# Kernel tuning notes

Measured on AMD Instinct MI355X. Metric: run time of the kernel, lower is better.

The kernel has to match this reference:

```python
import jax, jax.numpy as jnp
import numpy as np

N = 50000
E = 800000
NODE_F = 128
HID = 96
TEMP_F = 10


def setup_inputs() -> dict:
    key = jax.random.key(0)
    ks = jax.random.split(key, 10)
    x = jax.random.normal(ks[0], (N, NODE_F), dtype=jnp.float32)
    edge_index = jax.random.randint(ks[1], (2, E), 0, N, dtype=jnp.int64)
    temporal = jax.random.normal(ks[2], (N, TEMP_F), dtype=jnp.float32)
    # GCNConv: lin weight [in, out] (no bias in lin), separate bias [out]
    W_gcn = jax.random.normal(ks[3], (NODE_F, HID), dtype=jnp.float32) / np.sqrt(NODE_F)
    b_gcn = jnp.zeros((HID,), dtype=jnp.float32)
    W1 = jax.random.normal(ks[4], (HID + TEMP_F, HID), dtype=jnp.float32) / np.sqrt(HID + TEMP_F)
    b1 = jax.random.normal(ks[5], (HID,), dtype=jnp.float32) * 0.01
    W2 = jax.random.normal(ks[6], (HID + NODE_F, 1), dtype=jnp.float32) / np.sqrt(HID + NODE_F)
    b2 = jax.random.normal(ks[7], (1,), dtype=jnp.float32) * 0.01
    return {"x": x, "edge_index": edge_index, "temporal": temporal,
            "W_gcn": W_gcn, "b_gcn": b_gcn, "W1": W1, "b1": b1, "W2": W2, "b2": b2}


def _gcn_conv(x, edge_index, W, b):
    n = x.shape[0]
    loop = jnp.arange(n, dtype=edge_index.dtype)
    src = jnp.concatenate([edge_index[0], loop])  # [E+N]
    dst = jnp.concatenate([edge_index[1], loop])
    # symmetric normalization with self-loops (PyG gcn_norm)
    ones = jnp.ones(src.shape[0], dtype=x.dtype)
    deg = jax.ops.segment_sum(ones, dst, num_segments=n)
    dinv = jnp.where(deg > 0, jax.lax.rsqrt(deg), 0.0)
    norm = dinv[src] * dinv[dst]  # [E+N]
    h = x @ W  # [N, HID]
    msg = h[src] * norm[:, None]  # [E+N, HID] gather + scale
    out = jax.ops.segment_sum(msg, dst, num_segments=n)  # scatter-add
    return out + b


def reference(x, edge_index, temporal, W_gcn, b_gcn, W1, b1, W2, b2):
    h = jax.nn.relu(_gcn_conv(x, edge_index, W_gcn, b_gcn))  # [N, HID]
    h = jnp.concatenate([h, temporal], axis=-1)              # [N, HID+TEMP_F]
    h = jax.nn.relu(h @ W1 + b1)                             # [N, HID]
    h = jnp.concatenate([h, x], axis=-1)                     # [N, HID+NODE_F]
    return jax.nn.relu(h @ W2 + b2)                          # [N, 1]
```

## Files before the change

### kernel.cpp

```cpp
#include <hip/hip_runtime.h>
#include <hip/hip_bf16.h>

#define NN 50000
#define NPAD 50048
#define NE 800000
#define NF 128
#define HH 96
#define TF 10
#define Z1DIM (HH + TF)
#define ZK 128
#define NCH 4
#define CW 24
#define NBK 196
#define CAP 5120
#define EPB 8192

typedef __attribute__((ext_vector_type(8))) short short8;
typedef __attribute__((ext_vector_type(4))) float f32x4;

__device__ __forceinline__ float bu2f(unsigned short u) {
    union { unsigned int i; float f; } c;
    c.i = ((unsigned int)u) << 16;
    return c.f;
}
__device__ __forceinline__ unsigned short f2bu(float f) {
    union { __hip_bfloat16 h; unsigned short u; } c;
    c.h = __float2bfloat16(f);
    return c.u;
}

__global__ void k_init(int* __restrict__ bcur) {
    int t = threadIdx.x;
    if (t < NBK) bcur[t] = t * CAP;
}

__global__ __launch_bounds__(256) void k_fillA(const int* __restrict__ ei,
                                               int* __restrict__ bcur,
                                               int* __restrict__ temp) {
    __shared__ int hist[NBK], base[NBK];
    const int t = threadIdx.x;
    for (int m = t; m < NBK; m += 256) hist[m] = 0;
    __syncthreads();
    const int e0 = blockIdx.x * EPB;
    const int ecap = min(e0 + EPB, NE);
    for (int e = e0 + t; e < ecap; e += 256) {
        int d = ei[NE + e];
        atomicAdd(&hist[d >> 8], 1);
    }
    __syncthreads();
    for (int m = t; m < NBK; m += 256) {
        int c = hist[m];
        base[m] = c ? atomicAdd(&bcur[m], c) : 0;
        hist[m] = 0;
    }
    __syncthreads();
    for (int e = e0 + t; e < ecap; e += 256) {
        int d = ei[NE + e], s = ei[e];
        int b = d >> 8;
        int r = atomicAdd(&hist[b], 1);
        temp[base[b] + r] = ((d & 255) << 16) | s;
    }
}

__global__ __launch_bounds__(256) void k_gscan(const int* __restrict__ bcur,
                                               int* __restrict__ gbase) {
    __shared__ int p[256];
    const int t = threadIdx.x;
    int sz = (t < NBK) ? (bcur[t] - t * CAP) : 0;
    p[t] = sz;
    __syncthreads();
#pragma unroll
    for (int d = 1; d < 256; d <<= 1) {
        int u = (t >= d) ? p[t - d] : 0;
        __syncthreads();
        p[t] += u;
        __syncthreads();
    }
    if (t < NBK) gbase[t] = p[t] - sz;
}

__global__ __launch_bounds__(256) void k_fillB(const int* __restrict__ temp,
                                               const int* __restrict__ bcur,
                                               const int* __restrict__ gbase,
                                               int* __restrict__ csr,
                                               int* __restrict__ cnt,
                                               int* __restrict__ off,
                                               float* __restrict__ dinv) {
    __shared__ int ls[256], lc[256];
    const int b = blockIdx.x, t = threadIdx.x;
    const int seg0 = b * CAP;
    const int m = bcur[b] - seg0;
    const int g0 = gbase[b];
    ls[t] = 0;
    __syncthreads();
    for (int k = t; k < m; k += 256) atomicAdd(&ls[temp[seg0 + k] >> 16], 1);
    __syncthreads();
    const int myc = ls[t];
    lc[t] = myc;
    __syncthreads();
#pragma unroll
    for (int d = 1; d < 256; d <<= 1) {
        int u = (t >= d) ? lc[t - d] : 0;
        __syncthreads();
        lc[t] += u;
        __syncthreads();
    }
    const int myoff = lc[t] - myc;
    __syncthreads();
    lc[t] = myoff;
    const int i = b * 256 + t;
    if (i < NN) {
        cnt[i] = myc;
        off[i] = g0 + myoff;
        dinv[i] = rsqrtf((float)myc + 1.0f);
    }
    __syncthreads();
    for (int k = t; k < m; k += 256) {
        int v = temp[seg0 + k];
        int r = atomicAdd(&lc[v >> 16], 1);
        csr[g0 + r] = v & 0xFFFF;
    }
}

#define XBLK (NPAD * NF / 4 / 256)
#define WBLK (NF * HH / 4 / 256)
#define W1BLK (HH * ZK / 4 / 256)
__global__ void k_prep(const float* __restrict__ x, const float* __restrict__ W,
                       const float* __restrict__ W1,
                       unsigned short* __restrict__ xb, unsigned short* __restrict__ Wt,
                       unsigned short* __restrict__ Wt1) {
    int b = blockIdx.x;
    if (b < XBLK) {
        int idx4 = (b * 256 + threadIdx.x) * 4;
        int row = idx4 >> 7;
        ushort4 v;
        if (row < NN) {
            float4 f = *(const float4*)(x + idx4);
            v.x = f2bu(f.x); v.y = f2bu(f.y); v.z = f2bu(f.z); v.w = f2bu(f.w);
        } else {
            v.x = v.y = v.z = v.w = 0;
        }
        *(ushort4*)(xb + idx4) = v;
    } else if (b < XBLK + WBLK) {
        int e = ((b - XBLK) * 256 + threadIdx.x) * 4;
        int n = e >> 7, k = e & 127;
        ushort4 v;
        v.x = f2bu(W[(k + 0) * HH + n]);
        v.y = f2bu(W[(k + 1) * HH + n]);
        v.z = f2bu(W[(k + 2) * HH + n]);
        v.w = f2bu(W[(k + 3) * HH + n]);
        *(ushort4*)(Wt + e) = v;
    } else {
        int e = ((b - XBLK - WBLK) * 256 + threadIdx.x) * 4;
        int n = e >> 7, k = e & 127;
        ushort4 v;
        v.x = (k + 0 < Z1DIM) ? f2bu(W1[(k + 0) * HH + n]) : (unsigned short)0;
        v.y = (k + 1 < Z1DIM) ? f2bu(W1[(k + 1) * HH + n]) : (unsigned short)0;
        v.z = (k + 2 < Z1DIM) ? f2bu(W1[(k + 2) * HH + n]) : (unsigned short)0;
        v.w = (k + 3 < Z1DIM) ? f2bu(W1[(k + 3) * HH + n]) : (unsigned short)0;
        *(ushort4*)(Wt1 + e) = v;
    }
}

__global__ __launch_bounds__(256) void k_gemm(const unsigned short* __restrict__ xb,
                                              const unsigned short* __restrict__ Wt,
                                              const float* __restrict__ dinv,
                                              unsigned short* __restrict__ hp_c) {
    const int wave = threadIdx.x >> 6;
    const int lane = threadIdx.x & 63;
    const int quad = lane >> 4;
    const int l16 = lane & 15;
    const int Mbase = blockIdx.x * 64 + wave * 16;

    const unsigned short* arow = xb + (size_t)(Mbase + l16) * NF + quad * 8;
    const unsigned short* brow = Wt + (size_t)l16 * NF + quad * 8;

    f32x4 acc[6] = {};
#pragma unroll
    for (int ks = 0; ks < 4; ++ks) {
        short8 a = *(const short8*)(arow + ks * 32);
#pragma unroll
        for (int nt = 0; nt < 6; ++nt) {
            short8 bfrag = *(const short8*)(brow + (size_t)nt * 16 * NF + ks * 32);
            acc[nt] = __builtin_amdgcn_mfma_f32_16x16x32_bf16(a, bfrag, acc[nt], 0, 0, 0);
        }
    }
    const int r0 = Mbase + quad * 4;
    float dv0 = (r0 + 0 < NN) ? dinv[r0 + 0] : 0.f;
    float dv1 = (r0 + 1 < NN) ? dinv[r0 + 1] : 0.f;
    float dv2 = (r0 + 2 < NN) ? dinv[r0 + 2] : 0.f;
    float dv3 = (r0 + 3 < NN) ? dinv[r0 + 3] : 0.f;
#pragma unroll
    for (int nt = 0; nt < 6; ++nt) {
        int n = nt * 16 + l16;
        int c = n / CW, jj = n - c * CW;
        unsigned short* dst = hp_c + (size_t)c * NN * CW + jj;
        if (r0 + 0 < NN) dst[(size_t)(r0 + 0) * CW] = f2bu(acc[nt][0] * dv0);
        if (r0 + 1 < NN) dst[(size_t)(r0 + 1) * CW] = f2bu(acc[nt][1] * dv1);
        if (r0 + 2 < NN) dst[(size_t)(r0 + 2) * CW] = f2bu(acc[nt][2] * dv2);
        if (r0 + 3 < NN) dst[(size_t)(r0 + 3) * CW] = f2bu(acc[nt][3] * dv3);
    }
}

#define AGGT (NCH * NN * 6)
__global__ void k_agg(const unsigned short* __restrict__ hp_c,
                      const int* __restrict__ cnt, const int* __restrict__ off,
                      const int* __restrict__ csr, const float* __restrict__ dinv,
                      const float* __restrict__ bg,
                      unsigned short* __restrict__ zb) {
    int t = blockIdx.x * 256 + threadIdx.x;
    if (t >= AGGT) return;
    int c = t / (NN * 6);
    int rem = t - c * (NN * 6);
    int i = rem / 6;
    int q = rem - i * 6;
    const unsigned short* base = hp_c + (size_t)c * NN * CW + q * 4;

    ushort4 sv = *(const ushort4*)(base + (size_t)i * CW);
    float a0 = bu2f(sv.x), a1 = bu2f(sv.y), a2 = bu2f(sv.z), a3 = bu2f(sv.w);

    int idx = off[i];
    const int cdeg = cnt[i];
    const int end = idx + cdeg;
    for (; idx + 1 < end; idx += 2) {
        int s0 = csr[idx], s1 = csr[idx + 1];
        ushort4 v0 = *(const ushort4*)(base + (size_t)s0 * CW);
        ushort4 v1 = *(const ushort4*)(base + (size_t)s1 * CW);
        a0 += bu2f(v0.x) + bu2f(v1.x);
        a1 += bu2f(v0.y) + bu2f(v1.y);
        a2 += bu2f(v0.z) + bu2f(v1.z);
        a3 += bu2f(v0.w) + bu2f(v1.w);
    }
    if (idx < end) {
        ushort4 v0 = *(const ushort4*)(base + (size_t)csr[idx] * CW);
        a0 += bu2f(v0.x); a1 += bu2f(v0.y); a2 += bu2f(v0.z); a3 += bu2f(v0.w);
    }
    const float dv = dinv[i];
    const int j = c * CW + q * 4;
    ushort4 o;
    o.x = f2bu(fmaxf(fmaf(dv, a0, bg[j + 0]), 0.f));
    o.y = f2bu(fmaxf(fmaf(dv, a1, bg[j + 1]), 0.f));
    o.z = f2bu(fmaxf(fmaf(dv, a2, bg[j + 2]), 0.f));
    o.w = f2bu(fmaxf(fmaf(dv, a3, bg[j + 3]), 0.f));
    *(ushort4*)(zb + (size_t)i * ZK + j) = o;
}

#define ZTA (NPAD * 32)
#define ZTB ((NPAD - NN) * HH)
__global__ void k_ztail(const float* __restrict__ tmp, unsigned short* __restrict__ zb) {
    int t = blockIdx.x * 256 + threadIdx.x;
    if (t < ZTA) {
        int i = t >> 5, cc = t & 31;
        unsigned short v = 0;
        if (i < NN && cc < TF) v = f2bu(tmp[(size_t)i * TF + cc]);
        zb[(size_t)i * ZK + HH + cc] = v;
    } else {
        int u = t - ZTA;
        if (u < ZTB) {
            int i = NN + u / HH, j = u % HH;
            zb[(size_t)i * ZK + j] = 0;
        }
    }
}

__global__ __launch_bounds__(256) void k_mlp2(const unsigned short* __restrict__ zb,
                                              const unsigned short* __restrict__ Wt1,
                                              const float* __restrict__ b1,
                                              const float* __restrict__ W2,
                                              const float* __restrict__ b2,
                                              const float* __restrict__ x,
                                              float* __restrict__ out) {
    const int wave = threadIdx.x >> 6;
    const int lane = threadIdx.x & 63;
    const int quad = lane >> 4;
    const int l16 = lane & 15;
    const int Mbase = blockIdx.x * 64 + wave * 16;

    const unsigned short* arow = zb + (size_t)(Mbase + l16) * ZK + quad * 8;
    const unsigned short* brow = Wt1 + (size_t)l16 * ZK + quad * 8;

    f32x4 acc[6] = {};
#pragma unroll
    for (int ks = 0; ks < 4; ++ks) {
        short8 a = *(const short8*)(arow + ks * 32);
#pragma unroll
        for (int nt = 0; nt < 6; ++nt) {
            short8 bfrag = *(const short8*)(brow + (size_t)nt * 16 * ZK + ks * 32);
            acc[nt] = __builtin_amdgcn_mfma_f32_16x16x32_bf16(a, bfrag, acc[nt], 0, 0, 0);
        }
    }
    float bb[6], wa[6];
#pragma unroll
    for (int nt = 0; nt < 6; ++nt) {
        int c = nt * 16 + l16;
        bb[nt] = b1[c];
        wa[nt] = W2[c];
    }
    float wx[8];
#pragma unroll
    for (int m = 0; m < 8; ++m) wx[m] = W2[HH + l16 * 8 + m];
    const float bias2 = b2[0];

#pragma unroll
    for (int reg = 0; reg < 4; ++reg) {
        const int r = Mbase + quad * 4 + reg;
        float p = 0.f;
#pragma unroll
        for (int nt = 0; nt < 6; ++nt)
            p = fmaf(fmaxf(acc[nt][reg] + bb[nt], 0.f), wa[nt], p);
        if (r < NN) {
            const float4 xa = *(const float4*)(x + (size_t)r * NF + l16 * 8);
            const float4 xc = *(const float4*)(x + (size_t)r * NF + l16 * 8 + 4);
            p = fmaf(xa.x, wx[0], p); p = fmaf(xa.y, wx[1], p);
            p = fmaf(xa.z, wx[2], p); p = fmaf(xa.w, wx[3], p);
            p = fmaf(xc.x, wx[4], p); p = fmaf(xc.y, wx[5], p);
            p = fmaf(xc.z, wx[6], p); p = fmaf(xc.w, wx[7], p);
        }
#pragma unroll
        for (int m = 1; m < 16; m <<= 1) p += __shfl_xor(p, m, 64);
        if (l16 == 0 && r < NN) out[r] = fmaxf(p + bias2, 0.f);
    }
}

extern "C" void kernel_launch(void* const* d_in, const int* in_sizes, int n_in,
                              void* d_out, int out_size, void* d_ws, size_t ws_size,
                              hipStream_t stream) {
    const float* x   = (const float*)d_in[0];
    const int*   ei  = (const int*)d_in[1];
    const float* tmp = (const float*)d_in[2];
    const float* Wg  = (const float*)d_in[3];
    const float* bg  = (const float*)d_in[4];
    const float* W1  = (const float*)d_in[5];
    const float* b1  = (const float*)d_in[6];
    const float* W2  = (const float*)d_in[7];
    const float* b2  = (const float*)d_in[8];
    float* out = (float*)d_out;

    char* base = (char*)d_ws;
    int* cnt  = (int*)base;
    int* off  = cnt + 65536;
    int* bcur = off + 65536;
    int* gbase = bcur + 256;
    int* csr  = gbase + 256;
    float* dinv = (float*)(base + ((size_t)4 << 20));
    unsigned short* xb = (unsigned short*)(base + ((size_t)4 << 20) + 262144);
    unsigned short* Wt = xb + (size_t)NPAD * NF;
    unsigned short* hp_c = Wt + NF * HH;
    unsigned short* Wt1 = hp_c + (size_t)NN * HH;
    unsigned short* zb = Wt1 + HH * ZK;
    int* temp = (int*)zb;

    k_init <<<1, 256, 0, stream>>>(bcur);
    k_fillA<<<(NE + EPB - 1) / EPB, 256, 0, stream>>>(ei, bcur, temp);
    k_gscan<<<1, 256, 0, stream>>>(bcur, gbase);
    k_fillB<<<NBK, 256, 0, stream>>>(temp, bcur, gbase, csr, cnt, off, dinv);
    k_prep <<<XBLK + WBLK + W1BLK, 256, 0, stream>>>(x, Wg, W1, xb, Wt, Wt1);
    k_gemm <<<NPAD / 64, 256, 0, stream>>>(xb, Wt, dinv, hp_c);
    k_agg  <<<(AGGT + 255) / 256, 256, 0, stream>>>(hp_c, cnt, off, csr, dinv, bg, zb);
    k_ztail<<<(ZTA + ZTB + 255) / 256, 256, 0, stream>>>(tmp, zb);
    k_mlp2 <<<NPAD / 64, 256, 0, stream>>>(zb, Wt1, b1, W2, b2, x, out);
}
```

Measured before the change: 208.9 us.

## Widen aggregation gathers to 8 bf16, derive degree from offsets, fold tail fill

The aggregation kernel now has each thread gather 8 bf16 features (16-byte loads) per neighbour instead of 4, and blocks are interleaved across channel chunks. The neighbour index list and offsets are therefore read by half as many threads. The separate cnt and dinv arrays are removed: degree and rsqrt normalization are recomputed from consecutive CSR offsets, with a sentinel off[NN] written at init. The temporal-feature copy and pad-row zeroing from k_ztail are folded into k_prep, removing one launch. The cost is fewer threads for latency hiding in the gather and a redundant rsqrt in both the GEMM and the aggregation.

```diff
diff --git a/kernel.cpp b/kernel.cpp
--- a/kernel.cpp
+++ b/kernel.cpp
@@ -16,6 +16,7 @@
 #define EPB 8192
 
 typedef __attribute__((ext_vector_type(8))) short short8;
+typedef __attribute__((ext_vector_type(8))) unsigned short ushort8;
 typedef __attribute__((ext_vector_type(4))) float f32x4;
 
 __device__ __forceinline__ float bu2f(unsigned short u) {
@@ -29,9 +30,10 @@
     return c.u;
 }
 
-__global__ void k_init(int* __restrict__ bcur) {
+__global__ void k_init(int* __restrict__ bcur, int* __restrict__ off) {
     int t = threadIdx.x;
     if (t < NBK) bcur[t] = t * CAP;
+    if (t == 255) off[NN] = NE;
 }
 
 __global__ __launch_bounds__(256) void k_fillA(const int* __restrict__ ei,
@@ -83,9 +85,7 @@
                                                const int* __restrict__ bcur,
                                                const int* __restrict__ gbase,
                                                int* __restrict__ csr,
-                                               int* __restrict__ cnt,
-                                               int* __restrict__ off,
-                                               float* __restrict__ dinv) {
+                                               int* __restrict__ off) {
     __shared__ int ls[256], lc[256];
     const int b = blockIdx.x, t = threadIdx.x;
     const int seg0 = b * CAP;
@@ -109,11 +109,7 @@
     __syncthreads();
     lc[t] = myoff;
     const int i = b * 256 + t;
-    if (i < NN) {
-        cnt[i] = myc;
-        off[i] = g0 + myoff;
-        dinv[i] = rsqrtf((float)myc + 1.0f);
-    }
+    if (i < NN) off[i] = g0 + myoff;
     __syncthreads();
     for (int k = t; k < m; k += 256) {
         int v = temp[seg0 + k];
@@ -125,10 +121,12 @@
 #define XBLK (NPAD * NF / 4 / 256)
 #define WBLK (NF * HH / 4 / 256)
 #define W1BLK (HH * ZK / 4 / 256)
+#define ZTBLK (NPAD / 32)
+#define ZPBLK 5
 __global__ void k_prep(const float* __restrict__ x, const float* __restrict__ W,
-                       const float* __restrict__ W1,
+                       const float* __restrict__ W1, const float* __restrict__ tmp,
                        unsigned short* __restrict__ xb, unsigned short* __restrict__ Wt,
-                       unsigned short* __restrict__ Wt1) {
+                       unsigned short* __restrict__ Wt1, unsigned short* __restrict__ zb) {
     int b = blockIdx.x;
     if (b < XBLK) {
         int idx4 = (b * 256 + threadIdx.x) * 4;
@@ -150,7 +148,7 @@
         v.z = f2bu(W[(k + 2) * HH + n]);
         v.w = f2bu(W[(k + 3) * HH + n]);
         *(ushort4*)(Wt + e) = v;
-    } else {
+    } else if (b < XBLK + WBLK + W1BLK) {
         int e = ((b - XBLK - WBLK) * 256 + threadIdx.x) * 4;
         int n = e >> 7, k = e & 127;
         ushort4 v;
@@ -159,12 +157,30 @@
         v.z = (k + 2 < Z1DIM) ? f2bu(W1[(k + 2) * HH + n]) : (unsigned short)0;
         v.w = (k + 3 < Z1DIM) ? f2bu(W1[(k + 3) * HH + n]) : (unsigned short)0;
         *(ushort4*)(Wt1 + e) = v;
+    } else if (b < XBLK + WBLK + W1BLK + ZTBLK) {
+        int t4 = ((b - XBLK - WBLK - W1BLK) * 256 + threadIdx.x) * 4;
+        int i = t4 >> 5, cc = t4 & 31;
+        ushort4 v; v.x = v.y = v.z = v.w = 0;
+        if (i < NN) {
+            if (cc + 0 < TF) v.x = f2bu(tmp[(size_t)i * TF + cc + 0]);
+            if (cc + 1 < TF) v.y = f2bu(tmp[(size_t)i * TF + cc + 1]);
+            if (cc + 2 < TF) v.z = f2bu(tmp[(size_t)i * TF + cc + 2]);
+            if (cc + 3 < TF) v.w = f2bu(tmp[(size_t)i * TF + cc + 3]);
+        }
+        *(ushort4*)(zb + (size_t)i * ZK + HH + cc) = v;
+    } else {
+        int t4 = ((b - XBLK - WBLK - W1BLK - ZTBLK) * 256 + threadIdx.x) * 4;
+        if (t4 < (NPAD - NN) * HH) {
+            int i = NN + t4 / HH, j = t4 % HH;
+            ushort4 z; z.x = z.y = z.z = z.w = 0;
+            *(ushort4*)(zb + (size_t)i * ZK + j) = z;
+        }
     }
 }
 
 __global__ __launch_bounds__(256) void k_gemm(const unsigned short* __restrict__ xb,
                                               const unsigned short* __restrict__ Wt,
-                                              const float* __restrict__ dinv,
+                                              const int* __restrict__ off,
                                               unsigned short* __restrict__ hp_c) {
     const int wave = threadIdx.x >> 6;
     const int lane = threadIdx.x & 63;
@@ -186,81 +202,76 @@
         }
     }
     const int r0 = Mbase + quad * 4;
-    float dv0 = (r0 + 0 < NN) ? dinv[r0 + 0] : 0.f;
-    float dv1 = (r0 + 1 < NN) ? dinv[r0 + 1] : 0.f;
-    float dv2 = (r0 + 2 < NN) ? dinv[r0 + 2] : 0.f;
-    float dv3 = (r0 + 3 < NN) ? dinv[r0 + 3] : 0.f;
+    float dv[4];
+#pragma unroll
+    for (int k = 0; k < 4; ++k) {
+        int r = r0 + k;
+        dv[k] = (r < NN) ? rsqrtf((float)(off[r + 1] - off[r]) + 1.f) : 0.f;
+    }
 #pragma unroll
     for (int nt = 0; nt < 6; ++nt) {
         int n = nt * 16 + l16;
         int c = n / CW, jj = n - c * CW;
         unsigned short* dst = hp_c + (size_t)c * NN * CW + jj;
-        if (r0 + 0 < NN) dst[(size_t)(r0 + 0) * CW] = f2bu(acc[nt][0] * dv0);
-        if (r0 + 1 < NN) dst[(size_t)(r0 + 1) * CW] = f2bu(acc[nt][1] * dv1);
-        if (r0 + 2 < NN) dst[(size_t)(r0 + 2) * CW] = f2bu(acc[nt][2] * dv2);
-        if (r0 + 3 < NN) dst[(size_t)(r0 + 3) * CW] = f2bu(acc[nt][3] * dv3);
-    }
-}
-
-#define AGGT (NCH * NN * 6)
-__global__ void k_agg(const unsigned short* __restrict__ hp_c,
-                      const int* __restrict__ cnt, const int* __restrict__ off,
-                      const int* __restrict__ csr, const float* __restrict__ dinv,
-                      const float* __restrict__ bg,
-                      unsigned short* __restrict__ zb) {
-    int t = blockIdx.x * 256 + threadIdx.x;
-    if (t >= AGGT) return;
-    int c = t / (NN * 6);
-    int rem = t - c * (NN * 6);
-    int i = rem / 6;
-    int q = rem - i * 6;
-    const unsigned short* base = hp_c + (size_t)c * NN * CW + q * 4;
-
-    ushort4 sv = *(const ushort4*)(base + (size_t)i * CW);
-    float a0 = bu2f(sv.x), a1 = bu2f(sv.y), a2 = bu2f(sv.z), a3 = bu2f(sv.w);
+#pragma unroll
+        for (int k = 0; k < 4; ++k)
+            if (r0 + k < NN) dst[(size_t)(r0 + k) * CW] = f2bu(acc[nt][k] * dv[k]);
+    }
+}
+
+#define RPC 586
+#define AGGB (4 * RPC)
+__global__ __launch_bounds__(256) void k_agg(const unsigned short* __restrict__ hp_c,
+                                             const int* __restrict__ off,
+                                             const int* __restrict__ csr,
+                                             const float* __restrict__ bg,
+                                             unsigned short* __restrict__ zb) {
+    const int b = blockIdx.x;
+    const int slot = b & 7;
+    const int c = slot >> 1;
+    const int r = (b >> 3) * 2 + (slot & 1);
+    const int item = r * 256 + threadIdx.x;
+    if (item >= NN * 3) return;
+    const int i = item / 3;
+    const int q = item - i * 3;
+    const unsigned short* base = hp_c + (size_t)c * NN * CW + q * 8;
+
+    ushort8 sv = *(const ushort8*)(base + (size_t)i * CW);
+    float a0 = bu2f(sv[0]), a1 = bu2f(sv[1]), a2 = bu2f(sv[2]), a3 = bu2f(sv[3]);
+    float a4 = bu2f(sv[4]), a5 = bu2f(sv[5]), a6 = bu2f(sv[6]), a7 = bu2f(sv[7]);
 
     int idx = off[i];
-    const int cdeg = cnt[i];
-    const int end = idx + cdeg;
+    const int end = off[i + 1];
+    const float dv = rsqrtf((float)(end - idx) + 1.f);
     for (; idx + 1 < end; idx += 2) {
         int s0 = csr[idx], s1 = csr[idx + 1];
-        ushort4 v0 = *(const ushort4*)(base + (size_t)s0 * CW);
-        ushort4 v1 = *(const ushort4*)(base + (size_t)s1 * CW);
-        a0 += bu2f(v0.x) + bu2f(v1.x);
-        a1 += bu2f(v0.y) + bu2f(v1.y);
-        a2 += bu2f(v0.z) + bu2f(v1.z);
-        a3 += bu2f(v0.w) + bu2f(v1.w);
+        ushort8 v0 = *(const ushort8*)(base + (size_t)s0 * CW);
+        ushort8 v1 = *(const ushort8*)(base + (size_t)s1 * CW);
+        a0 += bu2f(v0[0]) + bu2f(v1[0]);
+        a1 += bu2f(v0[1]) + bu2f(v1[1]);
+        a2 += bu2f(v0[2]) + bu2f(v1[2]);
+        a3 += bu2f(v0[3]) + bu2f(v1[3]);
+        a4 += bu2f(v0[4]) + bu2f(v1[4]);
+        a5 += bu2f(v0[5]) + bu2f(v1[5]);
+        a6 += bu2f(v0[6]) + bu2f(v1[6]);
+        a7 += bu2f(v0[7]) + bu2f(v1[7]);
     }
     if (idx < end) {
-        ushort4 v0 = *(const ushort4*)(base + (size_t)csr[idx] * CW);
-        a0 += bu2f(v0.x); a1 += bu2f(v0.y); a2 += bu2f(v0.z); a3 += bu2f(v0.w);
-    }
-    const float dv = dinv[i];
-    const int j = c * CW + q * 4;
-    ushort4 o;
-    o.x = f2bu(fmaxf(fmaf(dv, a0, bg[j + 0]), 0.f));
-    o.y = f2bu(fmaxf(fmaf(dv, a1, bg[j + 1]), 0.f));
-    o.z = f2bu(fmaxf(fmaf(dv, a2, bg[j + 2]), 0.f));
-    o.w = f2bu(fmaxf(fmaf(dv, a3, bg[j + 3]), 0.f));
-    *(ushort4*)(zb + (size_t)i * ZK + j) = o;
-}
-
-#define ZTA (NPAD * 32)
-#define ZTB ((NPAD - NN) * HH)
-__global__ void k_ztail(const float* __restrict__ tmp, unsigned short* __restrict__ zb) {
-    int t = blockIdx.x * 256 + threadIdx.x;
-    if (t < ZTA) {
-        int i = t >> 5, cc = t & 31;
-        unsigned short v = 0;
-        if (i < NN && cc < TF) v = f2bu(tmp[(size_t)i * TF + cc]);
-        zb[(size_t)i * ZK + HH + cc] = v;
-    } else {
-        int u = t - ZTA;
-        if (u < ZTB) {
-            int i = NN + u / HH, j = u % HH;
-            zb[(size_t)i * ZK + j] = 0;
-        }
-    }
+        ushort8 v0 = *(const ushort8*)(base + (size_t)csr[idx] * CW);
+        a0 += bu2f(v0[0]); a1 += bu2f(v0[1]); a2 += bu2f(v0[2]); a3 += bu2f(v0[3]);
+        a4 += bu2f(v0[4]); a5 += bu2f(v0[5]); a6 += bu2f(v0[6]); a7 += bu2f(v0[7]);
+    }
+    const int j = c * CW + q * 8;
+    ushort8 o;
+    o[0] = f2bu(fmaxf(fmaf(dv, a0, bg[j + 0]), 0.f));
+    o[1] = f2bu(fmaxf(fmaf(dv, a1, bg[j + 1]), 0.f));
+    o[2] = f2bu(fmaxf(fmaf(dv, a2, bg[j + 2]), 0.f));
+    o[3] = f2bu(fmaxf(fmaf(dv, a3, bg[j + 3]), 0.f));
+    o[4] = f2bu(fmaxf(fmaf(dv, a4, bg[j + 4]), 0.f));
+    o[5] = f2bu(fmaxf(fmaf(dv, a5, bg[j + 5]), 0.f));
+    o[6] = f2bu(fmaxf(fmaf(dv, a6, bg[j + 6]), 0.f));
+    o[7] = f2bu(fmaxf(fmaf(dv, a7, bg[j + 7]), 0.f));
+    *(ushort8*)(zb + (size_t)i * ZK + j) = o;
 }
 
 __global__ __launch_bounds__(256) void k_mlp2(const unsigned short* __restrict__ zb,
@@ -337,12 +348,10 @@
     float* out = (float*)d_out;
 
     char* base = (char*)d_ws;
-    int* cnt  = (int*)base;
-    int* off  = cnt + 65536;
+    int* off  = (int*)base;
     int* bcur = off + 65536;
     int* gbase = bcur + 256;
     int* csr  = gbase + 256;
-    float* dinv = (float*)(base + ((size_t)4 << 20));
     unsigned short* xb = (unsigned short*)(base + ((size_t)4 << 20) + 262144);
     unsigned short* Wt = xb + (size_t)NPAD * NF;
     unsigned short* hp_c = Wt + NF * HH;
@@ -350,13 +359,12 @@
     unsigned short* zb = Wt1 + HH * ZK;
     int* temp = (int*)zb;
 
-    k_init <<<1, 256, 0, stream>>>(bcur);
+    k_init <<<1, 256, 0, stream>>>(bcur, off);
     k_fillA<<<(NE + EPB - 1) / EPB, 256, 0, stream>>>(ei, bcur, temp);
     k_gscan<<<1, 256, 0, stream>>>(bcur, gbase);
-    k_fillB<<<NBK, 256, 0, stream>>>(temp, bcur, gbase, csr, cnt, off, dinv);
-    k_prep <<<XBLK + WBLK + W1BLK, 256, 0, stream>>>(x, Wg, W1, xb, Wt, Wt1);
-    k_gemm <<<NPAD / 64, 256, 0, stream>>>(xb, Wt, dinv, hp_c);
-    k_agg  <<<(AGGT + 255) / 256, 256, 0, stream>>>(hp_c, cnt, off, csr, dinv, bg, zb);
-    k_ztail<<<(ZTA + ZTB + 255) / 256, 256, 0, stream>>>(tmp, zb);
+    k_fillB<<<NBK, 256, 0, stream>>>(temp, bcur, gbase, csr, off);
+    k_prep <<<XBLK + WBLK + W1BLK + ZTBLK + ZPBLK, 256, 0, stream>>>(x, Wg, W1, tmp, xb, Wt, Wt1, zb);
+    k_gemm <<<NPAD / 64, 256, 0, stream>>>(xb, Wt, off, hp_c);
+    k_agg  <<<AGGB, 256, 0, stream>>>(hp_c, off, csr, bg, zb);
     k_mlp2 <<<NPAD / 64, 256, 0, stream>>>(zb, Wt1, b1, W2, b2, x, out);
 }
```

New measurement: 195.3 us. 1.07x faster.
